# Kernel optimization log

Hardware: AMD Instinct MI355X
Metric: run time of the kernel (lower is better)

The kernel has to match this reference:

```python
import jax, jax.numpy as jnp
import numpy as np

EPS = 1e-5
DIM = 1024

def layer_norm(x, gamma, beta):
    mu = jnp.mean(x, axis=-1, keepdims=True)
    var = jnp.var(x, axis=-1, keepdims=True)
    return (x - mu) * jax.lax.rsqrt(var + EPS) * gamma + beta

def setup_inputs() -> dict:
    key = jax.random.key(0)
    k1, k2 = jax.random.split(key)
    return {
        "image_features": jax.random.normal(k1, (32, 1024, DIM), dtype=jnp.float32),
        "text_features": jax.random.normal(k2, (32, 512, DIM), dtype=jnp.float32),
        "gamma": jnp.ones((DIM,), dtype=jnp.float32),
        "beta": jnp.zeros((DIM,), dtype=jnp.float32),
    }

def reference(image_features, text_features, gamma, beta):
    scale = DIM ** (-0.5)
    image_norm = layer_norm(image_features, gamma, beta)   # [B, Ni, D]
    text_norm = layer_norm(text_features, gamma, beta)     # [B, Nt, D]
    # shared attention matrix, softmax only over text axis
    attn = jax.nn.softmax(jnp.einsum('bid,btd->bit', image_norm, text_norm) * scale, axis=-1)  # [B, Ni, Nt]
    image_attended = jnp.einsum('bit,btd->bid', attn, text_norm)   # [B, Ni, D]
    text_attended = jnp.einsum('bit,bid->btd', attn, image_norm)   # [B, Nt, D] (attn reused transposed, no re-softmax)
    return (image_features + image_attended, text_features + text_attended)
```

## Files before the change

kernel.cpp:

```cpp
#include <hip/hip_runtime.h>
#include <hip/hip_bf16.h>

#define B_  32
#define NI_ 1024
#define NT_ 512
#define D_  1024

typedef __attribute__((ext_vector_type(8))) short bf16x8;
typedef __attribute__((ext_vector_type(4))) float f32x4;

__device__ __forceinline__ ushort f2b(float f) {
  unsigned u = __builtin_bit_cast(unsigned, f);
  u = (u + 0x7FFFu + ((u >> 16) & 1u)) >> 16;
  return (ushort)u;
}


__global__ __launch_bounds__(256) void ln_bf16_kernel(
    const float* __restrict__ x, const float* __restrict__ gamma,
    const float* __restrict__ beta, ushort* __restrict__ out)
{
  const int row  = blockIdx.x * 4 + (threadIdx.x >> 6);
  const int lane = threadIdx.x & 63;
  const float* xr = x + (size_t)row * D_;
  float4 v[4];
  float s = 0.f, sq = 0.f;
#pragma unroll
  for (int q = 0; q < 4; ++q) {
    v[q] = *reinterpret_cast<const float4*>(xr + q * 256 + lane * 4);
    s  += v[q].x + v[q].y + v[q].z + v[q].w;
    sq += v[q].x*v[q].x + v[q].y*v[q].y + v[q].z*v[q].z + v[q].w*v[q].w;
  }
#pragma unroll
  for (int m = 1; m < 64; m <<= 1) {
    s  += __shfl_xor(s,  m);
    sq += __shfl_xor(sq, m);
  }
  const float mean = s * (1.f / D_);
  const float rstd = rsqrtf(sq * (1.f / D_) - mean * mean + 1e-5f);
  ushort* orow = out + (size_t)row * D_;
#pragma unroll
  for (int q = 0; q < 4; ++q) {
    const float4 g  = *reinterpret_cast<const float4*>(gamma + q * 256 + lane * 4);
    const float4 bt = *reinterpret_cast<const float4*>(beta  + q * 256 + lane * 4);
    ushort4 o;
    o.x = f2b((v[q].x - mean) * rstd * g.x + bt.x);
    o.y = f2b((v[q].y - mean) * rstd * g.y + bt.y);
    o.z = f2b((v[q].z - mean) * rstd * g.z + bt.z);
    o.w = f2b((v[q].w - mean) * rstd * g.w + bt.w);
    *reinterpret_cast<ushort4*>(orow + q * 256 + lane * 4) = o;
  }
}

__global__ __launch_bounds__(256) void transpose_bf16_kernel(
    const ushort* __restrict__ in, ushort* __restrict__ out, int R, int C)
{
  __shared__ ushort lds[64][68];
  const size_t nb = (size_t)blockIdx.z * (size_t)R * C;
  const ushort* ib = in + nb;
  ushort* ob = out + nb;
  const int c0 = blockIdx.x * 64, r0 = blockIdx.y * 64;
  const int t = threadIdx.x;
#pragma unroll
  for (int it = 0; it < 2; ++it) {
    const int r = (t >> 3) + 32 * it;
    const int c = (t & 7) * 8;
    uint4 val = *reinterpret_cast<const uint4*>(ib + (size_t)(r0 + r) * C + c0 + c);
    *reinterpret_cast<uint2*>(&lds[r][c])     = make_uint2(val.x, val.y);
    *reinterpret_cast<uint2*>(&lds[r][c + 4]) = make_uint2(val.z, val.w);
  }
  __syncthreads();
#pragma unroll
  for (int it = 0; it < 2; ++it) {
    const int c  = (t >> 3) + 32 * it;
    const int rb = (t & 7) * 8;
    union { ushort u[8]; uint4 v; } pk;
#pragma unroll
    for (int j = 0; j < 8; ++j) pk.u[j] = lds[rb + j][c];
    *reinterpret_cast<uint4*>(ob + (size_t)(c0 + c) * R + r0 + rb) = pk.v;
  }
}

__global__ __launch_bounds__(512) void qk_softmax_kernel(
    const ushort* __restrict__ qn,
    const ushort* __restrict__ kn,
    ushort* __restrict__ attn_it,
    ushort* __restrict__ attn_ti)
{
  __shared__ __align__(16) ushort Asm[2][64 * 32];
  __shared__ __align__(16) ushort Bsm[2][512 * 32];
  __shared__ __align__(16) float reds[64][8];

  const int bid = blockIdx.x;
  const int sid = (bid & 7) * 64 + (bid >> 3);
  const int b   = sid >> 4;
  const int i0  = (sid & 15) * 64;
  const int tid  = threadIdx.x;
  const int w    = tid >> 6;
  const int lane = tid & 63;
  const int lr   = lane & 15;
  const int g    = lane >> 4;

  const ushort* qb = qn + ((size_t)b * NI_ + i0) * D_;
  const ushort* kb = kn + (size_t)b * NT_ * D_;

  const int srow = tid >> 2;
  const int scol = (tid & 3) * 8;
  const int wp = (((tid >> 6) << 6) | (((tid >> 2) & 15) << 2)
                | ((tid & 3) ^ ((tid >> 3) & 3))) * 8;
  const int chunkLane = ((lane & 15) << 2) | ((lane >> 4) ^ ((lane >> 1) & 3));

  uint4 ra, rb0, rb1, rb2, rb3;
  auto LOAD = [&](int t) {
    const int ko = t * 32 + scol;
    if (tid < 256) ra = *reinterpret_cast<const uint4*>(qb + (size_t)srow * D_ + ko);
    rb0 = *reinterpret_cast<const uint4*>(kb + (size_t)(srow      ) * D_ + ko);
    rb1 = *reinterpret_cast<const uint4*>(kb + (size_t)(srow + 128) * D_ + ko);
    rb2 = *reinterpret_cast<const uint4*>(kb + (size_t)(srow + 256) * D_ + ko);
    rb3 = *reinterpret_cast<const uint4*>(kb + (size_t)(srow + 384) * D_ + ko);
  };
  auto WRITE = [&](int nb) {
    if (tid < 256) *reinterpret_cast<uint4*>(&Asm[nb][wp]) = ra;
    *reinterpret_cast<uint4*>(&Bsm[nb][wp        ]) = rb0;
    *reinterpret_cast<uint4*>(&Bsm[nb][wp +  4096]) = rb1;
    *reinterpret_cast<uint4*>(&Bsm[nb][wp +  8192]) = rb2;
    *reinterpret_cast<uint4*>(&Bsm[nb][wp + 12288]) = rb3;
  };

  f32x4 acc[4][4];
#pragma unroll
  for (int i = 0; i < 4; ++i)
#pragma unroll
    for (int j = 0; j < 4; ++j) acc[i][j] = (f32x4){0.f, 0.f, 0.f, 0.f};

  LOAD(0); WRITE(0); __syncthreads();
  const int nst = D_ / 32;
  int cur = 0;
  for (int t = 0; t < nst; ++t) {
    if (t + 1 < nst) LOAD(t + 1);
    const ushort* As = Asm[cur];
    const ushort* Bs = Bsm[cur];
    bf16x8 af[4], bf[4];
#pragma unroll
    for (int i = 0; i < 4; ++i)
      af[i] = *reinterpret_cast<const bf16x8*>(As + (i * 64 + chunkLane) * 8);
#pragma unroll
    for (int j = 0; j < 4; ++j)
      bf[j] = *reinterpret_cast<const bf16x8*>(Bs + ((w * 4 + j) * 64 + chunkLane) * 8);
#pragma unroll
    for (int i = 0; i < 4; ++i)
#pragma unroll
      for (int j = 0; j < 4; ++j)
        acc[i][j] = __builtin_amdgcn_mfma_f32_16x16x32_bf16(af[i], bf[j], acc[i][j], 0, 0, 0);
    __syncthreads();
    if (t + 1 < nst) WRITE(cur ^ 1);
    __syncthreads();
    cur ^= 1;
  }

  const float c1 = 0.03125f * 1.44269504f;

  float sm[4][4];
#pragma unroll
  for (int i = 0; i < 4; ++i)
#pragma unroll
    for (int r = 0; r < 4; ++r) sm[i][r] = 0.f;
#pragma unroll
  for (int i = 0; i < 4; ++i)
#pragma unroll
    for (int j = 0; j < 4; ++j)
#pragma unroll
      for (int r = 0; r < 4; ++r) {
        const float p = exp2f(acc[i][j][r] * c1);
        acc[i][j][r] = p;
        sm[i][r] += p;
      }
#pragma unroll
  for (int i = 0; i < 4; ++i)
#pragma unroll
    for (int r = 0; r < 4; ++r) {
      float s = sm[i][r];
      s += __shfl_xor(s, 1);
      s += __shfl_xor(s, 2);
      s += __shfl_xor(s, 4);
      s += __shfl_xor(s, 8);
      sm[i][r] = s;
    }
  if (lr == 0) {
#pragma unroll
    for (int i = 0; i < 4; ++i)
#pragma unroll
      for (int r = 0; r < 4; ++r) reds[i * 16 + g * 4 + r][w] = sm[i][r];
  }
  __syncthreads();
  float inv[4][4];
#pragma unroll
  for (int i = 0; i < 4; ++i)
#pragma unroll
    for (int r = 0; r < 4; ++r) {
      const int row = i * 16 + g * 4 + r;
      const float4 a0 = *reinterpret_cast<const float4*>(&reds[row][0]);
      const float4 a1 = *reinterpret_cast<const float4*>(&reds[row][4]);
      inv[i][r] = 1.f / (a0.x + a0.y + a0.z + a0.w + a1.x + a1.y + a1.z + a1.w);
    }

#pragma unroll
  for (int i = 0; i < 4; ++i) {
    const int rbase = i0 + i * 16 + g * 4;
#pragma unroll
    for (int j = 0; j < 4; ++j) {
      const int tcol = w * 64 + j * 16 + lr;
      ushort4 pk;
      pk.x = f2b(acc[i][j][0] * inv[i][0]);
      pk.y = f2b(acc[i][j][1] * inv[i][1]);
      pk.z = f2b(acc[i][j][2] * inv[i][2]);
      pk.w = f2b(acc[i][j][3] * inv[i][3]);
      ushort* it_p = attn_it + ((size_t)b * NI_ + rbase) * NT_ + tcol;
      it_p[0 * NT_] = pk.x;
      it_p[1 * NT_] = pk.y;
      it_p[2 * NT_] = pk.z;
      it_p[3 * NT_] = pk.w;
      *reinterpret_cast<ushort4*>(attn_ti + ((size_t)b * NT_ + tcol) * NI_ + rbase) = pk;
    }
  }
}

__global__ __launch_bounds__(256) void bt_gemm_add_kernel(
    const ushort* __restrict__ A,
    const ushort* __restrict__ Bm,
    const float* __restrict__ add,
    float* __restrict__ out,
    int M, int N, int K)
{
  __shared__ __align__(16) ushort Asm[2][128 * 32];
  __shared__ __align__(16) ushort Bsm[2][128 * 32];

  const int nwx = N >> 7, nwy = M >> 7;
  const int per = (nwx * nwy * B_) >> 3;
  const int sid = (blockIdx.x & 7) * per + (blockIdx.x >> 3);
  const int b   = sid / (nwx * nwy);
  const int rem = sid - b * (nwx * nwy);
  const int m0  = (rem / nwx) * 128;
  const int n0  = (rem % nwx) * 128;

  const int tid  = threadIdx.x;
  const int w    = tid >> 6;
  const int lane = tid & 63;
  const int lr   = lane & 15;
  const int g    = lane >> 4;

  const ushort* Ab = A  + ((size_t)b * M + m0) * K;
  const ushort* Bb = Bm + ((size_t)b * N + n0) * K;

  const int srow = tid >> 2;
  const int scol = (tid & 3) * 8;
  const int wp = (((tid >> 6) << 6) | (((tid >> 2) & 15) << 2)
                | ((tid & 3) ^ ((tid >> 3) & 3))) * 8;
  const int chunkLane = ((lane & 15) << 2) | ((lane >> 4) ^ ((lane >> 1) & 3));

  uint4 ra0, ra1, rbx0, rbx1;
  auto LOAD = [&](int t) {
    const int ko = t * 32 + scol;
    ra0  = *reinterpret_cast<const uint4*>(Ab + (size_t)(srow     ) * K + ko);
    ra1  = *reinterpret_cast<const uint4*>(Ab + (size_t)(srow + 64) * K + ko);
    rbx0 = *reinterpret_cast<const uint4*>(Bb + (size_t)(srow     ) * K + ko);
    rbx1 = *reinterpret_cast<const uint4*>(Bb + (size_t)(srow + 64) * K + ko);
  };
  auto WRITE = [&](int nb) {
    *reinterpret_cast<uint4*>(&Asm[nb][wp       ]) = ra0;
    *reinterpret_cast<uint4*>(&Asm[nb][wp + 2048]) = ra1;
    *reinterpret_cast<uint4*>(&Bsm[nb][wp       ]) = rbx0;
    *reinterpret_cast<uint4*>(&Bsm[nb][wp + 2048]) = rbx1;
  };

  f32x4 acc[4][4];
#pragma unroll
  for (int i = 0; i < 4; ++i)
#pragma unroll
    for (int j = 0; j < 4; ++j) acc[i][j] = (f32x4){0.f, 0.f, 0.f, 0.f};

  LOAD(0); WRITE(0); __syncthreads();
  const int nst = K / 32;
  int cur = 0;
  for (int t = 0; t < nst; ++t) {
    if (t + 1 < nst) LOAD(t + 1);
    const ushort* As = Asm[cur];
    const ushort* Bs = Bsm[cur];
    bf16x8 af[4], bf[4];
#pragma unroll
    for (int i = 0; i < 4; ++i)
      af[i] = *reinterpret_cast<const bf16x8*>(
          As + (((w >> 1) * 4 + i) * 64 + chunkLane) * 8);
#pragma unroll
    for (int j = 0; j < 4; ++j)
      bf[j] = *reinterpret_cast<const bf16x8*>(
          Bs + (((w & 1) * 4 + j) * 64 + chunkLane) * 8);
#pragma unroll
    for (int i = 0; i < 4; ++i)
#pragma unroll
      for (int j = 0; j < 4; ++j)
        acc[i][j] = __builtin_amdgcn_mfma_f32_16x16x32_bf16(af[i], bf[j], acc[i][j], 0, 0, 0);
    __syncthreads();
    if (t + 1 < nst) WRITE(cur ^ 1);
    __syncthreads();
    cur ^= 1;
  }

  const size_t ob = (size_t)b * M * N;
  const int rbase = m0 + (w >> 1) * 64 + g * 4;
#pragma unroll
  for (int i = 0; i < 4; ++i)
#pragma unroll
    for (int j = 0; j < 4; ++j) {
      const int c = n0 + (w & 1) * 64 + j * 16 + lr;
#pragma unroll
      for (int r = 0; r < 4; ++r) {
        const size_t idx = ob + (size_t)(rbase + i * 16 + r) * N + c;
        out[idx] = add[idx] + acc[i][j][r];
      }
    }
}

extern "C" void kernel_launch(void* const* d_in, const int* in_sizes, int n_in,
                              void* d_out, int out_size, void* d_ws, size_t ws_size,
                              hipStream_t stream) {
  const float* imgf  = (const float*)d_in[0];
  const float* txtf  = (const float*)d_in[1];
  const float* gamma = (const float*)d_in[2];
  const float* beta  = (const float*)d_in[3];

  float* out0 = (float*)d_out;
  float* out1 = out0 + (size_t)B_ * NI_ * D_;

  const size_t SZ = (size_t)B_ * NT_ * NI_ * 2;
  char* ws = (char*)d_ws;
  ushort* attn_ti = (ushort*)ws;
  ushort* attn_it = (ushort*)(ws + SZ);
  ushort* txnT    = (ushort*)(ws + 2 * SZ);
  ushort* imnT    = (ushort*)(ws + SZ);
  ushort* imn     = (ushort*)out1;
  ushort* txn     = (ushort*)out0;

  ln_bf16_kernel<<<(B_ * NI_) / 4, 256, 0, stream>>>(imgf, gamma, beta, imn);
  ln_bf16_kernel<<<(B_ * NT_) / 4, 256, 0, stream>>>(txtf, gamma, beta, txn);
  qk_softmax_kernel<<<(NI_ / 64) * B_, 512, 0, stream>>>(imn, txn, attn_it, attn_ti);
  transpose_bf16_kernel<<<dim3(D_ / 64, NT_ / 64, B_), 256, 0, stream>>>(txn, txnT, NT_, D_);
  bt_gemm_add_kernel<<<(D_ / 128) * (NI_ / 128) * B_, 256, 0, stream>>>(
      attn_it, txnT, imgf, out0, NI_, D_, NT_);
  transpose_bf16_kernel<<<dim3(D_ / 64, NI_ / 64, B_), 256, 0, stream>>>(imn, imnT, NI_, D_);
  bt_gemm_add_kernel<<<(D_ / 128) * (NT_ / 128) * B_, 256, 0, stream>>>(
      attn_ti, imnT, txtf, out1, NT_, D_, NI_);
}
```

Before: 320.0 us.

## Use 256x256 tiles with direct global-to-LDS loads and split-phase MFMA pipeline

The two output GEMMs move to 256x256 tiles with 512 threads. Tiles are now staged through global_load_lds, so data goes straight into shared memory instead of passing through registers, and explicit vmcnt waits and barriers interleave the B and A prefetches with two half-steps of MFMA work. s_setprio is raised around the MFMA blocks. The aim is more operand reuse per tile and fewer register round trips for loads, at the cost of higher register pressure (8x4 accumulators), fewer blocks, and an LDS layout without the previous swizzle, which may cause bank conflicts.

```diff
diff --git a/kernel.cpp b/kernel.cpp
--- a/kernel.cpp
+++ b/kernel.cpp
@@ -15,6 +15,13 @@
   return (ushort)u;
 }
 
+__device__ __forceinline__ void gll16(const ushort* g, ushort* l) {
+  __builtin_amdgcn_global_load_lds(
+      (const __attribute__((address_space(1))) void*)g,
+      (__attribute__((address_space(3))) void*)l, 16, 0, 0);
+}
+
+#define VMWAIT(N) asm volatile("s_waitcnt vmcnt(" #N ")" ::: "memory")
 
 __global__ __launch_bounds__(256) void ln_bf16_kernel(
     const float* __restrict__ x, const float* __restrict__ gamma,
@@ -225,98 +232,110 @@
   }
 }
 
-__global__ __launch_bounds__(256) void bt_gemm_add_kernel(
+__global__ __launch_bounds__(512) void bt_gemm_add_kernel(
     const ushort* __restrict__ A,
     const ushort* __restrict__ Bm,
     const float* __restrict__ add,
     float* __restrict__ out,
     int M, int N, int K)
 {
-  __shared__ __align__(16) ushort Asm[2][128 * 32];
-  __shared__ __align__(16) ushort Bsm[2][128 * 32];
-
-  const int nwx = N >> 7, nwy = M >> 7;
+  __shared__ __align__(16) ushort Asm[2][256 * 32];
+  __shared__ __align__(16) ushort Bsm[2][256 * 32];
+
+  const int nwx = N >> 8, nwy = M >> 8;
   const int per = (nwx * nwy * B_) >> 3;
   const int sid = (blockIdx.x & 7) * per + (blockIdx.x >> 3);
   const int b   = sid / (nwx * nwy);
   const int rem = sid - b * (nwx * nwy);
-  const int m0  = (rem / nwx) * 128;
-  const int n0  = (rem % nwx) * 128;
+  const int m0  = (rem / nwx) * 256;
+  const int n0  = (rem % nwx) * 256;
 
   const int tid  = threadIdx.x;
   const int w    = tid >> 6;
   const int lane = tid & 63;
   const int lr   = lane & 15;
   const int g    = lane >> 4;
+  const int wm   = w >> 2;
+  const int wn   = w & 3;
 
   const ushort* Ab = A  + ((size_t)b * M + m0) * K;
   const ushort* Bb = Bm + ((size_t)b * N + n0) * K;
-
-  const int srow = tid >> 2;
-  const int scol = (tid & 3) * 8;
-  const int wp = (((tid >> 6) << 6) | (((tid >> 2) & 15) << 2)
-                | ((tid & 3) ^ ((tid >> 3) & 3))) * 8;
-  const int chunkLane = ((lane & 15) << 2) | ((lane >> 4) ^ ((lane >> 1) & 3));
-
-  uint4 ra0, ra1, rbx0, rbx1;
-  auto LOAD = [&](int t) {
-    const int ko = t * 32 + scol;
-    ra0  = *reinterpret_cast<const uint4*>(Ab + (size_t)(srow     ) * K + ko);
-    ra1  = *reinterpret_cast<const uint4*>(Ab + (size_t)(srow + 64) * K + ko);
-    rbx0 = *reinterpret_cast<const uint4*>(Bb + (size_t)(srow     ) * K + ko);
-    rbx1 = *reinterpret_cast<const uint4*>(Bb + (size_t)(srow + 64) * K + ko);
+  const int nst = K >> 5;
+
+  auto GLL_A = [&](int nb, int kt, int rb) {
+    gll16(Ab + (size_t)(rb * 16 + lr) * K + kt * 32 + g * 8,
+          &Asm[nb][rb * 64 * 8]);
   };
-  auto WRITE = [&](int nb) {
-    *reinterpret_cast<uint4*>(&Asm[nb][wp       ]) = ra0;
-    *reinterpret_cast<uint4*>(&Asm[nb][wp + 2048]) = ra1;
-    *reinterpret_cast<uint4*>(&Bsm[nb][wp       ]) = rbx0;
-    *reinterpret_cast<uint4*>(&Bsm[nb][wp + 2048]) = rbx1;
+  auto GLL_B = [&](int nb, int kt, int rb) {
+    gll16(Bb + (size_t)(rb * 16 + lr) * K + kt * 32 + g * 8,
+          &Bsm[nb][rb * 64 * 8]);
   };
-
-  f32x4 acc[4][4];
-#pragma unroll
-  for (int i = 0; i < 4; ++i)
+  const int rbA0 = (w & 3) + ((w >> 2) << 3);
+
+  f32x4 acc[8][4];
+#pragma unroll
+  for (int i = 0; i < 8; ++i)
 #pragma unroll
     for (int j = 0; j < 4; ++j) acc[i][j] = (f32x4){0.f, 0.f, 0.f, 0.f};
 
-  LOAD(0); WRITE(0); __syncthreads();
-  const int nst = K / 32;
-  int cur = 0;
+  GLL_B(0, 0, w); GLL_B(0, 0, w + 8);
+  GLL_A(0, 0, rbA0); GLL_A(0, 0, rbA0 + 4);
+
   for (int t = 0; t < nst; ++t) {
-    if (t + 1 < nst) LOAD(t + 1);
-    const ushort* As = Asm[cur];
-    const ushort* Bs = Bsm[cur];
-    bf16x8 af[4], bf[4];
-#pragma unroll
-    for (int i = 0; i < 4; ++i)
-      af[i] = *reinterpret_cast<const bf16x8*>(
-          As + (((w >> 1) * 4 + i) * 64 + chunkLane) * 8);
+    const int par = t & 1;
+    const ushort* As = Asm[par];
+    const ushort* Bs = Bsm[par];
+
+    VMWAIT(1);
+    __builtin_amdgcn_sched_barrier(0);
+    __builtin_amdgcn_s_barrier();
+
+    bf16x8 bf[4], af[4];
 #pragma unroll
     for (int j = 0; j < 4; ++j)
-      bf[j] = *reinterpret_cast<const bf16x8*>(
-          Bs + (((w & 1) * 4 + j) * 64 + chunkLane) * 8);
+      bf[j] = *reinterpret_cast<const bf16x8*>(Bs + ((wn * 4 + j) * 64 + lane) * 8);
+#pragma unroll
+    for (int i = 0; i < 4; ++i)
+      af[i] = *reinterpret_cast<const bf16x8*>(As + ((wm * 8 + i) * 64 + lane) * 8);
+    if (t + 1 < nst) { GLL_B(par ^ 1, t + 1, w); GLL_B(par ^ 1, t + 1, w + 8); }
+    __builtin_amdgcn_s_barrier();
+    __builtin_amdgcn_s_setprio(1);
 #pragma unroll
     for (int i = 0; i < 4; ++i)
 #pragma unroll
       for (int j = 0; j < 4; ++j)
         acc[i][j] = __builtin_amdgcn_mfma_f32_16x16x32_bf16(af[i], bf[j], acc[i][j], 0, 0, 0);
-    __syncthreads();
-    if (t + 1 < nst) WRITE(cur ^ 1);
-    __syncthreads();
-    cur ^= 1;
+    __builtin_amdgcn_s_setprio(0);
+
+    if (t + 1 < nst) { VMWAIT(2); } else { VMWAIT(0); }
+    __builtin_amdgcn_sched_barrier(0);
+    __builtin_amdgcn_s_barrier();
+
+#pragma unroll
+    for (int i = 0; i < 4; ++i)
+      af[i] = *reinterpret_cast<const bf16x8*>(As + ((wm * 8 + 4 + i) * 64 + lane) * 8);
+    if (t + 1 < nst) { GLL_A(par ^ 1, t + 1, rbA0); GLL_A(par ^ 1, t + 1, rbA0 + 4); }
+    __builtin_amdgcn_s_barrier();
+    __builtin_amdgcn_s_setprio(1);
+#pragma unroll
+    for (int i = 0; i < 4; ++i)
+#pragma unroll
+      for (int j = 0; j < 4; ++j)
+        acc[4 + i][j] = __builtin_amdgcn_mfma_f32_16x16x32_bf16(af[i], bf[j], acc[4 + i][j], 0, 0, 0);
+    __builtin_amdgcn_s_setprio(0);
   }
 
   const size_t ob = (size_t)b * M * N;
-  const int rbase = m0 + (w >> 1) * 64 + g * 4;
-#pragma unroll
-  for (int i = 0; i < 4; ++i)
+#pragma unroll
+  for (int hi = 0; hi < 8; ++hi)
 #pragma unroll
     for (int j = 0; j < 4; ++j) {
-      const int c = n0 + (w & 1) * 64 + j * 16 + lr;
+      const int mrow = m0 + wm * 128 + hi * 16 + g * 4;
+      const int c    = n0 + wn * 64 + j * 16 + lr;
 #pragma unroll
       for (int r = 0; r < 4; ++r) {
-        const size_t idx = ob + (size_t)(rbase + i * 16 + r) * N + c;
-        out[idx] = add[idx] + acc[i][j][r];
+        const size_t idx = ob + (size_t)(mrow + r) * N + c;
+        out[idx] = add[idx] + acc[hi][j][r];
       }
     }
 }
@@ -345,9 +364,9 @@
   ln_bf16_kernel<<<(B_ * NT_) / 4, 256, 0, stream>>>(txtf, gamma, beta, txn);
   qk_softmax_kernel<<<(NI_ / 64) * B_, 512, 0, stream>>>(imn, txn, attn_it, attn_ti);
   transpose_bf16_kernel<<<dim3(D_ / 64, NT_ / 64, B_), 256, 0, stream>>>(txn, txnT, NT_, D_);
-  bt_gemm_add_kernel<<<(D_ / 128) * (NI_ / 128) * B_, 256, 0, stream>>>(
+  bt_gemm_add_kernel<<<(D_ / 256) * (NI_ / 256) * B_, 512, 0, stream>>>(
       attn_it, txnT, imgf, out0, NI_, D_, NT_);
   transpose_bf16_kernel<<<dim3(D_ / 64, NI_ / 64, B_), 256, 0, stream>>>(imn, imnT, NI_, D_);
-  bt_gemm_add_kernel<<<(D_ / 128) * (NT_ / 128) * B_, 256, 0, stream>>>(
+  bt_gemm_add_kernel<<<(D_ / 256) * (NT_ / 256) * B_, 512, 0, stream>>>(
       attn_ti, imnT, txtf, out1, NT_, D_, NI_);
 }
```

After: 319.2 us. About the same (-0.2%).
